# Kernel optimization log

Measured on AMD Instinct MI355X. Metric: run time of the kernel, lower is better.

Reference implementation:

```python
import jax, jax.numpy as jnp
import numpy as np
from jax import lax

B, SEQ, CIN = 8, 4096, 7
DM, NL, PL = 512, 4, 16
NP = SEQ // PL            # 256 patches
NS, DC, EXP = 16, 4, 2
DI = EXP * DM             # 1024 inner dim
DTR = (DM + 15) // 16     # 32 dt_rank (mamba_ssm default ceil(d_model/16))
CD, PRED = 64, 96
EPS = 1e-5


def setup_inputs() -> dict:
    key = jax.random.key(0)
    ks = jax.random.split(key, 16)
    r = lambda k, s, sc=0.02: jax.random.normal(k, s, jnp.float32) * sc
    A_row = jnp.arange(1, NS + 1, dtype=jnp.float32)
    return {
        "x": jax.random.normal(ks[0], (B, SEQ, CIN), jnp.float32),
        "in_g": jnp.ones((CIN,), jnp.float32), "in_b": jnp.zeros((CIN,), jnp.float32),
        "pe_W": r(ks[1], (DM, CIN, PL), 0.1), "pe_b": jnp.zeros((DM,), jnp.float32),
        "ln_g": jnp.ones((NL, DM), jnp.float32), "ln_b": jnp.zeros((NL, DM), jnp.float32),
        "W_in": r(ks[2], (NL, 2 * DI, DM)),
        "conv_W": r(ks[3], (NL, DI, 1, DC), 0.2), "conv_b": jnp.zeros((NL, DI), jnp.float32),
        "W_x": r(ks[4], (NL, DTR + 2 * NS, DI)),
        "W_dt": r(ks[5], (NL, DI, DTR), 0.1),
        "b_dt": jnp.full((NL, DI), -4.6, jnp.float32),  # softplus^-1(~0.01)
        "A_log": jnp.log(jnp.tile(A_row, (NL, DI, 1))),
        "Dskip": jnp.ones((NL, DI), jnp.float32),
        "W_out": r(ks[6], (NL, DM, DI)),
        "fn_g": jnp.ones((DM,), jnp.float32), "fn_b": jnp.zeros((DM,), jnp.float32),
        "hW1": r(ks[7], (2 * CD, DM * NP)), "hb1": jnp.zeros((2 * CD,), jnp.float32),
        "hW2": r(ks[8], (PRED, 2 * CD)), "hb2": jnp.zeros((PRED,), jnp.float32),
    }


def layernorm(x, g, b):
    m = jnp.mean(x, axis=-1, keepdims=True)
    v = jnp.mean((x - m) ** 2, axis=-1, keepdims=True)
    return (x - m) * lax.rsqrt(v + EPS) * g + b


def silu(x):
    return x * jax.nn.sigmoid(x)


def selective_scan(dA, dBx, C):
    # dA, dBx: (B, L, DI, N);  C: (B, L, N)  ->  y: (B, L, DI)
    def step(h, t):
        dA_t, dbx_t, c_t = t
        h = dA_t * h + dbx_t                      # (B, DI, N)
        y = jnp.einsum('bdn,bn->bd', h, c_t)
        return h, y
    h0 = jnp.zeros((dA.shape[0], DI, NS), dA.dtype)
    _, ys = lax.scan(step, h0, (dA.transpose(1, 0, 2, 3), dBx.transpose(1, 0, 2, 3), C.transpose(1, 0, 2)))
    return ys.transpose(1, 0, 2)


def mamba_block(u, W_in, cW, cb, W_x, W_dt, b_dt, A_log, Dv, W_out):
    xz = jnp.einsum('bld,ed->ble', u, W_in)       # (B, L, 2*DI)
    xi, z = jnp.split(xz, 2, axis=-1)
    # causal depthwise conv over time
    xc = lax.conv_general_dilated(xi.transpose(0, 2, 1), cW, (1,), [(DC - 1, 0)],
                                  feature_group_count=DI,
                                  dimension_numbers=('NCH', 'OIH', 'NCH'))
    xc = silu(xc + cb[None, :, None]).transpose(0, 2, 1)  # (B, L, DI)
    dbl = jnp.einsum('bld,ed->ble', xc, W_x)      # (B, L, DTR + 2*NS)
    dt, Bm, Cm = dbl[..., :DTR], dbl[..., DTR:DTR + NS], dbl[..., DTR + NS:]
    delta = jax.nn.softplus(jnp.einsum('blr,dr->bld', dt, W_dt) + b_dt)  # (B, L, DI)
    A = -jnp.exp(A_log)                           # (DI, NS)
    dA = jnp.exp(delta[..., None] * A)            # (B, L, DI, NS)
    dBx = delta[..., None] * Bm[:, :, None, :] * xc[..., None]
    y = selective_scan(dA, dBx, Cm)
    y = (y + xc * Dv) * silu(z)
    return jnp.einsum('bld,od->blo', y, W_out)


def reference(x, in_g, in_b, pe_W, pe_b, ln_g, ln_b, W_in, conv_W, conv_b,
              W_x, W_dt, b_dt, A_log, Dskip, W_out, fn_g, fn_b, hW1, hb1, hW2, hb2):
    h = layernorm(x, in_g, in_b)
    # patch embed: stride==kernel Conv1d == per-patch matmul
    p = h.reshape(B, NP, PL, CIN)
    h = jnp.einsum('bnpc,dcp->bnd', p, pe_W) + pe_b   # (B, NP, DM)
    for i in range(NL):
        res = h
        h = layernorm(h, ln_g[i], ln_b[i])
        h = mamba_block(h, W_in[i], conv_W[i], conv_b[i], W_x[i], W_dt[i],
                        b_dt[i], A_log[i], Dskip[i], W_out[i])
        h = h + res                                   # dropout is identity at eval
    h = layernorm(h, fn_g, fn_b)
    h = h.reshape(B, -1)                              # (B, DM*NP)
    h = jax.nn.gelu(h @ hW1.T + hb1, approximate=False)
    return h @ hW2.T + hb2                            # (B, PRED)
```

## Files before the change

### kernel.cpp

```cpp
#include <hip/hip_runtime.h>
#include <hip/hip_bf16.h>
#include <math.h>

#define B_    8
#define SEQ_  4096
#define CIN_  7
#define DM_   512
#define NL_   4
#define PL_   16
#define NP_   256
#define NS_   16
#define DC_   4
#define DI_   1024
#define DTR_  32
#define CD_   64
#define PRED_ 96
#define TOK_  (B_*NP_)
#define KTOT_ (DM_*NP_)
#define EPS_  1e-5f
#define CL_   16
#define NCH_  (NP_/CL_)

typedef unsigned short u16;
typedef __attribute__((ext_vector_type(8))) short short8;
typedef __attribute__((ext_vector_type(4))) float floatx4;

__device__ __forceinline__ float silu_f(float x){ return x / (1.f + __expf(-x)); }
__device__ __forceinline__ float softplus_f(float x){ return x > 20.f ? x : log1pf(__expf(x)); }
__device__ __forceinline__ u16 f2bf(float f){
  union { __hip_bfloat16 h; u16 u; } cv; cv.h = __float2bfloat16(f); return cv.u;
}
__device__ __forceinline__ float bf2f(u16 u){
  union { unsigned int i; float f; } cv; cv.i = ((unsigned int)u) << 16; return cv.f;
}
#define GLDS16(g, l) __builtin_amdgcn_global_load_lds( \
    (const __attribute__((address_space(1))) void*)(g), \
    (__attribute__((address_space(3))) void*)(l), 16, 0, 0)

__global__ void ln7_kernel(const float* __restrict__ x, const float* __restrict__ g,
                           const float* __restrict__ b, u16* __restrict__ xpb){
  int i = blockIdx.x*256 + threadIdx.x;
  if (i >= B_*SEQ_) return;
  float v[CIN_]; float m = 0.f;
  #pragma unroll
  for (int c=0;c<CIN_;c++){ v[c]=x[i*CIN_+c]; m+=v[c]; }
  m *= (1.f/CIN_);
  float var = 0.f;
  #pragma unroll
  for (int c=0;c<CIN_;c++){ float d=v[c]-m; var+=d*d; }
  var *= (1.f/CIN_);
  float r = rsqrtf(var + EPS_);
  int bn = i >> 4, p = i & 15;
  u16* row = xpb + (size_t)bn*128;
  #pragma unroll
  for (int c=0;c<CIN_;c++) row[c*16+p] = f2bf((v[c]-m)*r*g[c]+b[c]);
  row[112+p] = 0;
}

__global__ __launch_bounds__(256) void ln512_kernel(const float* __restrict__ in,
    const float* __restrict__ g, const float* __restrict__ b, u16* __restrict__ outb){
  int tid = threadIdx.x;
  int wv = tid>>6, lane = tid&63;
  int t = blockIdx.x*4 + wv;
  const float4* row = (const float4*)(in + (size_t)t*DM_);
  float4 v0 = row[lane], v1 = row[64+lane];
  float s = v0.x+v0.y+v0.z+v0.w + v1.x+v1.y+v1.z+v1.w;
  #pragma unroll
  for (int o=1;o<64;o<<=1) s += __shfl_xor(s,o);
  float m = s*(1.f/DM_);
  float d0x=v0.x-m,d0y=v0.y-m,d0z=v0.z-m,d0w=v0.w-m;
  float d1x=v1.x-m,d1y=v1.y-m,d1z=v1.z-m,d1w=v1.w-m;
  float q = d0x*d0x+d0y*d0y+d0z*d0z+d0w*d0w + d1x*d1x+d1y*d1y+d1z*d1z+d1w*d1w;
  #pragma unroll
  for (int o=1;o<64;o<<=1) q += __shfl_xor(q,o);
  float r = rsqrtf(q*(1.f/DM_) + EPS_);
  float4 g0 = ((const float4*)g)[lane], g1 = ((const float4*)g)[64+lane];
  float4 b0 = ((const float4*)b)[lane], b1 = ((const float4*)b)[64+lane];
  float4 o0 = { d0x*r*g0.x+b0.x, d0y*r*g0.y+b0.y, d0z*r*g0.z+b0.z, d0w*r*g0.w+b0.w };
  float4 o1 = { d1x*r*g1.x+b1.x, d1y*r*g1.y+b1.y, d1z*r*g1.z+b1.z, d1w*r*g1.w+b1.w };
  ushort4 p0 = { f2bf(o0.x), f2bf(o0.y), f2bf(o0.z), f2bf(o0.w) };
  ushort4 p1 = { f2bf(o1.x), f2bf(o1.y), f2bf(o1.z), f2bf(o1.w) };
  ((ushort4*)(outb + (size_t)t*DM_))[lane]    = p0;
  ((ushort4*)(outb + (size_t)t*DM_))[64+lane] = p1;
}

template<int BM, int BN, bool ACC, bool BIAS>
__global__ __launch_bounds__(256) void gemm_bf16(const u16* __restrict__ A,
    const u16* __restrict__ Bw, float* __restrict__ C, const float* __restrict__ bias,
    int K, int lda, int ldb, int ldc){
  constexpr int MI = BM/32, NI = BN/32;
  __shared__ __align__(16) u16 As[BM*64];
  __shared__ __align__(16) u16 Bs[BN*64];
  int tid = threadIdx.x;
  int wave = __builtin_amdgcn_readfirstlane(tid>>6);
  int lane = tid&63;
  int wm = wave>>1, wn = wave&1;
  int quad = lane>>4, l16 = lane&15;
  int bm = blockIdx.y*BM, bn = blockIdx.x*BN;
  int r8 = lane>>3, sseg = lane&7;
  int gseg = sseg ^ r8;
  floatx4 acc[MI][NI] = {};
  for (int k0 = 0; k0 < K; k0 += 64){
    #pragma unroll
    for (int r = 0; r < BM/32; r++){
      int rowb = (r*4 + wave)*8;
      const u16* gp = A + (size_t)(bm + rowb + r8)*lda + k0 + gseg*8;
      GLDS16(gp, &As[rowb*64]);
    }
    #pragma unroll
    for (int r = 0; r < BN/32; r++){
      int rowb = (r*4 + wave)*8;
      const u16* gp = Bw + (size_t)(bn + rowb + r8)*ldb + k0 + gseg*8;
      GLDS16(gp, &Bs[rowb*64]);
    }
    __syncthreads();
    #pragma unroll
    for (int kh = 0; kh < 2; kh++){
      short8 af[MI], bfr[NI];
      #pragma unroll
      for (int i = 0; i < MI; i++){
        int row = wm*(BM/2)+i*16+l16;
        af[i] = *(short8*)&As[row*64 + (((kh*4+quad)^(row&7))*8)];
      }
      #pragma unroll
      for (int j = 0; j < NI; j++){
        int row = wn*(BN/2)+j*16+l16;
        bfr[j] = *(short8*)&Bs[row*64 + (((kh*4+quad)^(row&7))*8)];
      }
      #pragma unroll
      for (int i = 0; i < MI; i++)
        #pragma unroll
        for (int j = 0; j < NI; j++)
          acc[i][j] = __builtin_amdgcn_mfma_f32_16x16x32_bf16(af[i], bfr[j], acc[i][j], 0, 0, 0);
    }
    __syncthreads();
  }
  #pragma unroll
  for (int i = 0; i < MI; i++){
    #pragma unroll
    for (int j = 0; j < NI; j++){
      #pragma unroll
      for (int r = 0; r < 4; r++){
        int m  = bm + wm*(BM/2) + i*16 + quad*4 + r;
        int nn = bn + wn*(BN/2) + j*16 + l16;
        float v = acc[i][j][r];
        if (ACC) C[(size_t)m*ldc+nn] += v;
        else     C[(size_t)m*ldc+nn]  = BIAS ? v + bias[nn] : v;
      }
    }
  }
}

__global__ __launch_bounds__(256) void dblpart_kernel(const u16* __restrict__ A,
    const u16* __restrict__ Bw, float* __restrict__ part){
  __shared__ __align__(16) u16 As[64*64];
  __shared__ __align__(16) u16 Bs[64*64];
  int tid = threadIdx.x;
  int wave = __builtin_amdgcn_readfirstlane(tid>>6);
  int lane = tid&63;
  int wm = wave>>1, wn = wave&1;
  int quad = lane>>4, l16 = lane&15;
  int bm = blockIdx.x*64;
  int kc = blockIdx.y;
  int r8 = lane>>3, sseg = lane&7;
  int gseg = sseg ^ r8;
  floatx4 acc[2][2] = {};
  for (int k0 = kc*256; k0 < kc*256 + 256; k0 += 64){
    #pragma unroll
    for (int r = 0; r < 2; r++){
      int rowb = (r*4 + wave)*8;
      GLDS16(A  + (size_t)(bm + rowb + r8)*DI_ + k0 + gseg*8, &As[rowb*64]);
      GLDS16(Bw + (size_t)(     rowb + r8)*DI_ + k0 + gseg*8, &Bs[rowb*64]);
    }
    __syncthreads();
    #pragma unroll
    for (int kh = 0; kh < 2; kh++){
      short8 af[2], bfr[2];
      #pragma unroll
      for (int i = 0; i < 2; i++){
        int row = wm*32+i*16+l16;
        af[i] = *(short8*)&As[row*64 + (((kh*4+quad)^(row&7))*8)];
      }
      #pragma unroll
      for (int j = 0; j < 2; j++){
        int row = wn*32+j*16+l16;
        bfr[j] = *(short8*)&Bs[row*64 + (((kh*4+quad)^(row&7))*8)];
      }
      #pragma unroll
      for (int i = 0; i < 2; i++)
        #pragma unroll
        for (int j = 0; j < 2; j++)
          acc[i][j] = __builtin_amdgcn_mfma_f32_16x16x32_bf16(af[i], bfr[j], acc[i][j], 0, 0, 0);
    }
    __syncthreads();
  }
  float* dst = part + (size_t)kc*TOK_*64;
  #pragma unroll
  for (int i = 0; i < 2; i++)
    #pragma unroll
    for (int j = 0; j < 2; j++)
      #pragma unroll
      for (int r = 0; r < 4; r++){
        int m  = bm + wm*32 + i*16 + quad*4 + r;
        int nn = wn*32 + j*16 + l16;
        dst[(size_t)m*64+nn] = acc[i][j][r];
      }
}

__global__ void conv_silu_kernel(const float* __restrict__ xz, const float* __restrict__ cW,
                                 const float* __restrict__ cb, u16* __restrict__ xcb){
  int idx = blockIdx.x*256 + threadIdx.x;
  if (idx >= TOK_*DI_/4) return;
  int c4 = idx & (DI_/4 - 1); int t = idx >> 8;
  int l = t & (NP_-1);
  int c = c4*4;
  float4 acc = *(const float4*)&cb[c];
  float wa[4], wb[4], wc[4], wd[4];
  *(float4*)wa = *(const float4*)&cW[(c+0)*DC_];
  *(float4*)wb = *(const float4*)&cW[(c+1)*DC_];
  *(float4*)wc = *(const float4*)&cW[(c+2)*DC_];
  *(float4*)wd = *(const float4*)&cW[(c+3)*DC_];
  const float* base = xz + (size_t)t*(2*DI_) + c;
  #pragma unroll
  for (int k = 0; k < DC_; k++){
    if (l - 3 + k >= 0){
      float4 xv = *(const float4*)(base + (k-3)*(2*DI_));
      acc.x += xv.x*wa[k];
      acc.y += xv.y*wb[k];
      acc.z += xv.z*wc[k];
      acc.w += xv.w*wd[k];
    }
  }
  ushort4 pb = { f2bf(silu_f(acc.x)), f2bf(silu_f(acc.y)),
                 f2bf(silu_f(acc.z)), f2bf(silu_f(acc.w)) };
  *(ushort4*)&xcb[(size_t)t*DI_ + c] = pb;
}

__global__ __launch_bounds__(256) void delta_kernel(const float* __restrict__ part,
    const float* __restrict__ wdtT, const float* __restrict__ bdt,
    float* __restrict__ dbl, float* __restrict__ delta){
  __shared__ float sdt[16][DTR_];
  int tid = threadIdx.x;
  int t0 = blockIdx.y*16;
  int dx = blockIdx.x;
  int d = dx*256 + tid;
  for (int i = tid; i < 16*32; i += 256){
    int t = i >> 5, r = i & 31;
    size_t o = (size_t)(t0 + t)*64 + r;
    sdt[t][r] = part[o] + part[(size_t)TOK_*64 + o]
              + part[(size_t)2*TOK_*64 + o] + part[(size_t)3*TOK_*64 + o];
  }
  if (dx == 0){
    for (int i = tid; i < 16*32; i += 256){
      int t = i >> 5, c = i & 31;
      size_t o = (size_t)(t0 + t)*64 + 32 + c;
      dbl[o] = part[o] + part[(size_t)TOK_*64 + o]
             + part[(size_t)2*TOK_*64 + o] + part[(size_t)3*TOK_*64 + o];
    }
  }
  float wv[DTR_];
  #pragma unroll
  for (int r = 0; r < DTR_; r++) wv[r] = wdtT[(size_t)r*DI_ + d];
  float bb = bdt[d];
  __syncthreads();
  #pragma unroll 4
  for (int t = 0; t < 16; t++){
    float acc = bb;
    #pragma unroll
    for (int r = 0; r < DTR_; r++) acc += sdt[t][r]*wv[r];
    delta[(size_t)(t0 + t)*DI_ + d] = softplus_f(acc);
  }
}

__global__ __launch_bounds__(256) void scan_part_kernel(const float* __restrict__ delta,
    const u16* __restrict__ xcb, const float* __restrict__ dbl,
    const float* __restrict__ Alog, float* __restrict__ hend, float* __restrict__ aprod){
  __shared__ float sBC[CL_][32];
  int tid = threadIdx.x;
  int d = blockIdx.x*256 + tid;
  int bych = blockIdx.y;
  int b = bych >> 4, ch = bych & (NCH_-1);
  int base = b*NP_ + ch*CL_;
  for (int i = tid; i < CL_*32; i += 256){
    int t = i >> 5, c = i & 31;
    sBC[t][c] = dbl[(size_t)(base+t)*64 + 32 + c];
  }
  float A[NS_], h[NS_], pr[NS_];
  #pragma unroll
  for (int k = 0; k < NS_; k++){
    A[k] = -__expf(Alog[(size_t)d*NS_ + k]);
    h[k] = 0.f; pr[k] = 1.f;
  }
  __syncthreads();
  #pragma unroll
  for (int t = 0; t < CL_; t++){
    int row = base + t;
    float de = delta[(size_t)row*DI_ + d];
    float xv = bf2f(xcb[(size_t)row*DI_ + d]);
    float cde = de*xv;
    #pragma unroll
    for (int k = 0; k < NS_; k++){
      float a = __expf(de*A[k]);
      h[k] = a*h[k] + cde*sBC[t][k];
      pr[k] *= a;
    }
  }
  size_t o = ((size_t)bych*DI_ + d)*NS_;
  #pragma unroll
  for (int k = 0; k < NS_; k++){ hend[o+k] = h[k]; aprod[o+k] = pr[k]; }
}

__global__ __launch_bounds__(256) void scan_fix_kernel(const float* __restrict__ aprod,
    float* __restrict__ hend){
  int id = blockIdx.x*256 + threadIdx.x;
  int nd = id & (DI_*NS_ - 1);
  int b  = id >> 14;
  float h = 0.f;
  #pragma unroll
  for (int ch = 0; ch < NCH_; ch++){
    size_t idx = (size_t)(b*NCH_ + ch)*(DI_*NS_) + nd;
    float ap = aprod[idx];
    float he = hend[idx];
    hend[idx] = h;
    h = ap*h + he;
  }
}

__global__ __launch_bounds__(256) void scan_final_kernel(const float* __restrict__ delta,
    const u16* __restrict__ xcb, const float* __restrict__ dbl,
    const float* __restrict__ xz, const float* __restrict__ Dv,
    const float* __restrict__ Alog, const float* __restrict__ hin,
    u16* __restrict__ yb){
  __shared__ float sBC[CL_][32];
  int tid = threadIdx.x;
  int d = blockIdx.x*256 + tid;
  int bych = blockIdx.y;
  int b = bych >> 4, ch = bych & (NCH_-1);
  int base = b*NP_ + ch*CL_;
  for (int i = tid; i < CL_*32; i += 256){
    int t = i >> 5, c = i & 31;
    sBC[t][c] = dbl[(size_t)(base+t)*64 + 32 + c];
  }
  float A[NS_], h[NS_];
  size_t o = ((size_t)bych*DI_ + d)*NS_;
  #pragma unroll
  for (int k = 0; k < NS_; k++){
    A[k] = -__expf(Alog[(size_t)d*NS_ + k]);
    h[k] = hin[o + k];
  }
  float Dvd = Dv[d];
  __syncthreads();
  #pragma unroll
  for (int t = 0; t < CL_; t++){
    int row = base + t;
    float de = delta[(size_t)row*DI_ + d];
    float xv = bf2f(xcb[(size_t)row*DI_ + d]);
    float zz = xz[(size_t)row*(2*DI_) + DI_ + d];
    float cde = de*xv;
    float p = 0.f;
    #pragma unroll
    for (int k = 0; k < NS_; k++){
      float a = __expf(de*A[k]);
      h[k] = a*h[k] + cde*sBC[t][k];
      p += h[k]*sBC[t][16+k];
    }
    yb[(size_t)row*DI_ + d] = f2bf((p + xv*Dvd) * silu_f(zz));
  }
}

__global__ __launch_bounds__(256) void head1_kernel(const float* __restrict__ hW1,
    const u16* __restrict__ ub, float* __restrict__ partial){
  __shared__ __align__(16) u16 As[128*64];
  __shared__ __align__(16) u16 Bs[16*64];
  int tid = threadIdx.x;
  int wave = __builtin_amdgcn_readfirstlane(tid>>6);
  int lane = tid & 63, quad = lane>>4, l16 = lane&15;
  int kc = blockIdx.x;
  int arow = tid & 127, apair = tid >> 7;
  floatx4 acc[2] = {};
  for (int sc = 0; sc < 4; sc++){
    int k0 = kc*256 + sc*64;
    const float* ap = hW1 + (size_t)arow*KTOT_ + k0 + apair*32;
    #pragma unroll
    for (int s = 0; s < 4; s++){
      float4 f0 = *(const float4*)(ap + s*8);
      float4 f1 = *(const float4*)(ap + s*8 + 4);
      union { u16 h[8]; int4 v; } pk;
      pk.h[0]=f2bf(f0.x); pk.h[1]=f2bf(f0.y); pk.h[2]=f2bf(f0.z); pk.h[3]=f2bf(f0.w);
      pk.h[4]=f2bf(f1.x); pk.h[5]=f2bf(f1.y); pk.h[6]=f2bf(f1.z); pk.h[7]=f2bf(f1.w);
      int seg = apair*4 + s;
      *(int4*)&As[arow*64 + ((seg^(arow&7))*8)] = pk.v;
    }
    if (tid < 128){
      int brow = tid >> 3, bseg = tid & 7;
      int4 bv = {0,0,0,0};
      if (brow < 8) bv = *(const int4*)&ub[(size_t)brow*KTOT_ + k0 + bseg*8];
      *(int4*)&Bs[brow*64 + ((bseg^(brow&7))*8)] = bv;
    }
    __syncthreads();
    #pragma unroll
    for (int kh = 0; kh < 2; kh++){
      short8 bf = *(short8*)&Bs[l16*64 + (((kh*4+quad)^(l16&7))*8)];
      #pragma unroll
      for (int i = 0; i < 2; i++){
        int row = wave*32 + i*16 + l16;
        short8 af = *(short8*)&As[row*64 + (((kh*4+quad)^(row&7))*8)];
        acc[i] = __builtin_amdgcn_mfma_f32_16x16x32_bf16(af, bf, acc[i], 0, 0, 0);
      }
    }
    __syncthreads();
  }
  if (l16 < 8){
    #pragma unroll
    for (int i = 0; i < 2; i++)
      #pragma unroll
      for (int r = 0; r < 4; r++){
        int n = wave*32 + i*16 + quad*4 + r;
        partial[(size_t)kc*1024 + n*8 + l16] = acc[i][r];
      }
  }
}

__global__ void head_comb1_kernel(const float* __restrict__ partial, float* __restrict__ pp2){
  int out = blockIdx.x*256 + threadIdx.x;
  int g = blockIdx.y;
  const float* p = partial + (size_t)g*64*1024 + out;
  float s = 0.f;
  #pragma unroll 8
  for (int j = 0; j < 64; j++) s += p[(size_t)j*1024];
  pp2[g*1024 + out] = s;
}

__global__ void head_comb2_kernel(const float* __restrict__ pp2,
    const float* __restrict__ hb1, float* __restrict__ t1){
  int out = blockIdx.x*256 + threadIdx.x;
  int n = out >> 3, m = out & 7;
  float s = hb1[n];
  #pragma unroll
  for (int g = 0; g < 8; g++) s += pp2[g*1024 + out];
  float ge = 0.5f*s*(1.f + erff(s*0.70710678118f));
  t1[m*128 + n] = ge;
}

__global__ void head2_kernel(const float* __restrict__ t1, const float* __restrict__ hW2,
                             const float* __restrict__ hb2, float* __restrict__ out){
  int idx = blockIdx.x*128 + threadIdx.x;
  if (idx >= B_*PRED_) return;
  int m = idx / PRED_, q = idx % PRED_;
  float s = hb2[q];
  #pragma unroll 16
  for (int k = 0; k < 2*CD_; k++) s += t1[m*128 + k]*hW2[q*128 + k];
  out[idx] = s;
}

__global__ __launch_bounds__(256) void prep_kernel(const float* __restrict__ W_dt,
    const float* __restrict__ W_x, const float* __restrict__ W_in,
    const float* __restrict__ W_out, const float* __restrict__ peW,
    float* __restrict__ wdtT, u16* __restrict__ wxB,
    u16* __restrict__ WinB, u16* __restrict__ WoutB, u16* __restrict__ peWb){
  int idx = blockIdx.x*256 + threadIdx.x;
  {
    float4 v = ((const float4*)W_in)[idx];
    ushort4 o = { f2bf(v.x), f2bf(v.y), f2bf(v.z), f2bf(v.w) };
    ((ushort4*)WinB)[idx] = o;
  }
  if (idx < 524288){
    float4 v = ((const float4*)W_out)[idx];
    ushort4 o = { f2bf(v.x), f2bf(v.y), f2bf(v.z), f2bf(v.w) };
    ((ushort4*)WoutB)[idx] = o;
  }
  if (idx < NL_*64*DI_/4){
    float4 v = ((const float4*)W_x)[idx];
    ushort4 o = { f2bf(v.x), f2bf(v.y), f2bf(v.z), f2bf(v.w) };
    ((ushort4*)wxB)[idx] = o;
  }
  if (idx < NL_*DTR_*DI_){
    int l = idx / (DTR_*DI_); int rem = idx % (DTR_*DI_);
    int r = rem / DI_; int d = rem % DI_;
    wdtT[idx] = W_dt[((size_t)l*DI_ + d)*DTR_ + r];
  }
  if (idx < 512*128){
    int d = idx >> 7, kk = idx & 127;
    peWb[idx] = (kk < 112) ? f2bf(peW[d*112 + kk]) : (u16)0;
  }
}

extern "C" void kernel_launch(void* const* d_in, const int* in_sizes, int n_in,
                              void* d_out, int out_size, void* d_ws, size_t ws_size,
                              hipStream_t stream) {
  const float* x      = (const float*)d_in[0];
  const float* in_g   = (const float*)d_in[1];
  const float* in_b   = (const float*)d_in[2];
  const float* pe_W   = (const float*)d_in[3];
  const float* pe_b   = (const float*)d_in[4];
  const float* ln_g   = (const float*)d_in[5];
  const float* ln_b   = (const float*)d_in[6];
  const float* W_in   = (const float*)d_in[7];
  const float* conv_W = (const float*)d_in[8];
  const float* conv_b = (const float*)d_in[9];
  const float* W_x    = (const float*)d_in[10];
  const float* W_dt   = (const float*)d_in[11];
  const float* b_dt   = (const float*)d_in[12];
  const float* A_log  = (const float*)d_in[13];
  const float* Dskip  = (const float*)d_in[14];
  const float* W_out  = (const float*)d_in[15];
  const float* fn_g   = (const float*)d_in[16];
  const float* fn_b   = (const float*)d_in[17];
  const float* hW1    = (const float*)d_in[18];
  const float* hb1    = (const float*)d_in[19];
  const float* hW2    = (const float*)d_in[20];
  const float* hb2    = (const float*)d_in[21];

  float* ws    = (float*)d_ws;
  float* h     = ws;
  float* un    = h     + 1048576;
  float* xz    = un    + 1048576;
  float* xc    = xz    + 4194304;
  float* dblb  = xc    + 2097152;
  float* delta = dblb  + 131072;
  float* y     = delta + 2097152;
  float* wdtT  = y     + 2097152;
  u16*   wxB   = (u16*)(wdtT + 131072);
  float* bf_rgn= wdtT + 131072 + 131072;
  u16*   unb   = (u16*)bf_rgn;
  u16*   yb    = (u16*)(bf_rgn + 524288);
  u16*   WinB  = (u16*)(bf_rgn + 524288 + 1048576);
  u16*   WoutB = (u16*)(bf_rgn + 524288 + 1048576 + 2097152);
  u16*   peWb  = (u16*)(bf_rgn + 524288 + 1048576 + 2097152 + 1048576);
  float* aprod = bf_rgn + 524288 + 1048576 + 2097152 + 1048576 + 32768;
  float* hend  = y;
  u16*   xcb   = (u16*)xc;
  u16*   xpb   = (u16*)y;
  float* dblpart = aprod;
  float* partial = xz;
  float* pp2     = xz + 524288;
  float* t1      = xz + 532480;

  prep_kernel<<<4096, 256, 0, stream>>>(W_dt, W_x, W_in, W_out, pe_W,
                                        wdtT, wxB, WinB, WoutB, peWb);
  ln7_kernel<<<(B_*SEQ_+255)/256, 256, 0, stream>>>(x, in_g, in_b, xpb);
  gemm_bf16<64,128,false,true><<<dim3(DM_/128, TOK_/64), 256, 0, stream>>>(
      xpb, peWb, h, pe_b, 128, 128, 128, DM_);

  for (int l = 0; l < NL_; l++){
    ln512_kernel<<<TOK_/4, 256, 0, stream>>>(h, ln_g + l*DM_, ln_b + l*DM_, unb);
    gemm_bf16<64,128,false,false><<<dim3(2*DI_/128, TOK_/64), 256, 0, stream>>>(
        unb, WinB + (size_t)l*2*DI_*DM_, xz, nullptr, DM_, DM_, DM_, 2*DI_);
    conv_silu_kernel<<<(TOK_*DI_/4)/256, 256, 0, stream>>>(
        xz, conv_W + (size_t)l*DI_*DC_, conv_b + (size_t)l*DI_, xcb);
    dblpart_kernel<<<dim3(TOK_/64, 4), 256, 0, stream>>>(
        xcb, wxB + (size_t)l*64*DI_, dblpart);
    delta_kernel<<<dim3(DI_/256, TOK_/16), 256, 0, stream>>>(
        dblpart, wdtT + (size_t)l*DTR_*DI_, b_dt + (size_t)l*DI_, dblb, delta);
    scan_part_kernel<<<dim3(DI_/256, B_*NCH_), 256, 0, stream>>>(
        delta, xcb, dblb, A_log + (size_t)l*DI_*NS_, hend, aprod);
    scan_fix_kernel<<<(B_*DI_*NS_)/256, 256, 0, stream>>>(aprod, hend);
    scan_final_kernel<<<dim3(DI_/256, B_*NCH_), 256, 0, stream>>>(
        delta, xcb, dblb, xz, Dskip + (size_t)l*DI_, A_log + (size_t)l*DI_*NS_, hend, yb);
    gemm_bf16<64,64,true,false><<<dim3(DM_/64, TOK_/64), 256, 0, stream>>>(
        yb, WoutB + (size_t)l*DM_*DI_, h, nullptr, DI_, DI_, DI_, DM_);
  }

  ln512_kernel<<<TOK_/4, 256, 0, stream>>>(h, fn_g, fn_b, unb);
  head1_kernel<<<512, 256, 0, stream>>>(hW1, unb, partial);
  head_comb1_kernel<<<dim3(4, 8), 256, 0, stream>>>(partial, pp2);
  head_comb2_kernel<<<4, 256, 0, stream>>>(pp2, hb1, t1);
  head2_kernel<<<6, 128, 0, stream>>>(t1, hW2, hb2, (float*)d_out);
}
```

Baseline: 553.1 us.

## Fuse conv+SiLU into x_proj GEMM and delta projection into chunk scan

Computes the causal depthwise conv and SiLU directly into the shared-memory A tile of the x_proj partial GEMM, so the block no longer reloads xc from global. The delta projection is merged into the first chunked-scan pass, keeping delta in registers instead of re-reading it. It also widens the in_proj GEMM M tile to 128 and moves the dblpart buffer to a different scratch region. Together these remove two launches per layer and some global round trips, at the cost of larger shared memory per block and more registers.

```diff
diff --git a/kernel.cpp b/kernel.cpp
--- a/kernel.cpp
+++ b/kernel.cpp
@@ -151,39 +151,83 @@
   }
 }
 
-__global__ __launch_bounds__(256) void dblpart_kernel(const u16* __restrict__ A,
-    const u16* __restrict__ Bw, float* __restrict__ part){
-  __shared__ __align__(16) u16 As[64*64];
+__global__ __launch_bounds__(256) void convdbl_kernel(const float* __restrict__ xz,
+    const float* __restrict__ cW, const float* __restrict__ cb,
+    const u16* __restrict__ wxB, u16* __restrict__ xcb, float* __restrict__ part){
+  __shared__ __align__(16) u16 As[64*256];
   __shared__ __align__(16) u16 Bs[64*64];
   int tid = threadIdx.x;
+  int t0 = blockIdx.x*64;
+  int kc = blockIdx.y;
+  int cbase = kc*256;
+  {
+    int cg = tid & 31;
+    int tq = tid >> 5;
+    int c = cbase + cg*8;
+    float wt[8][4], bias[8];
+    #pragma unroll
+    for (int j = 0; j < 8; j++){
+      float4 w4 = *(const float4*)&cW[(size_t)(c+j)*DC_];
+      wt[j][0]=w4.x; wt[j][1]=w4.y; wt[j][2]=w4.z; wt[j][3]=w4.w;
+    }
+    float4 bq0 = *(const float4*)&cb[c], bq1 = *(const float4*)&cb[c+4];
+    bias[0]=bq0.x; bias[1]=bq0.y; bias[2]=bq0.z; bias[3]=bq0.w;
+    bias[4]=bq1.x; bias[5]=bq1.y; bias[6]=bq1.z; bias[7]=bq1.w;
+    #pragma unroll
+    for (int r = 0; r < 8; r++){
+      int trow = t0 + r*8 + tq;
+      int l = trow & (NP_-1);
+      float a[8];
+      #pragma unroll
+      for (int j = 0; j < 8; j++) a[j] = bias[j];
+      #pragma unroll
+      for (int tap = 0; tap < DC_; tap++){
+        if (l + tap >= 3){
+          const float* px = xz + (size_t)(trow + tap - 3)*(2*DI_) + c;
+          float4 x0 = *(const float4*)px;
+          float4 x1 = *(const float4*)(px + 4);
+          a[0]+=x0.x*wt[0][tap]; a[1]+=x0.y*wt[1][tap];
+          a[2]+=x0.z*wt[2][tap]; a[3]+=x0.w*wt[3][tap];
+          a[4]+=x1.x*wt[4][tap]; a[5]+=x1.y*wt[5][tap];
+          a[6]+=x1.z*wt[6][tap]; a[7]+=x1.w*wt[7][tap];
+        }
+      }
+      union { u16 h[8]; int4 v; } pk;
+      #pragma unroll
+      for (int j = 0; j < 8; j++) pk.h[j] = f2bf(silu_f(a[j]));
+      int trel = trow - t0;
+      *(int4*)&As[trel*256 + ((cg ^ (trel&7))*8)] = pk.v;
+      *(int4*)&xcb[(size_t)trow*DI_ + c] = pk.v;
+    }
+  }
+  __syncthreads();
   int wave = __builtin_amdgcn_readfirstlane(tid>>6);
   int lane = tid&63;
   int wm = wave>>1, wn = wave&1;
   int quad = lane>>4, l16 = lane&15;
-  int bm = blockIdx.x*64;
-  int kc = blockIdx.y;
   int r8 = lane>>3, sseg = lane&7;
   int gseg = sseg ^ r8;
   floatx4 acc[2][2] = {};
-  for (int k0 = kc*256; k0 < kc*256 + 256; k0 += 64){
+  for (int sc = 0; sc < 4; sc++){
+    int k0 = cbase + sc*64;
     #pragma unroll
     for (int r = 0; r < 2; r++){
       int rowb = (r*4 + wave)*8;
-      GLDS16(A  + (size_t)(bm + rowb + r8)*DI_ + k0 + gseg*8, &As[rowb*64]);
-      GLDS16(Bw + (size_t)(     rowb + r8)*DI_ + k0 + gseg*8, &Bs[rowb*64]);
+      GLDS16(wxB + (size_t)(rowb + r8)*DI_ + k0 + gseg*8, &Bs[rowb*64]);
     }
     __syncthreads();
     #pragma unroll
     for (int kh = 0; kh < 2; kh++){
+      int lseg = sc*8 + kh*4 + quad;
       short8 af[2], bfr[2];
       #pragma unroll
       for (int i = 0; i < 2; i++){
-        int row = wm*32+i*16+l16;
-        af[i] = *(short8*)&As[row*64 + (((kh*4+quad)^(row&7))*8)];
+        int row = wm*32 + i*16 + l16;
+        af[i] = *(short8*)&As[row*256 + ((lseg ^ (row&7))*8)];
       }
       #pragma unroll
       for (int j = 0; j < 2; j++){
-        int row = wn*32+j*16+l16;
+        int row = wn*32 + j*16 + l16;
         bfr[j] = *(short8*)&Bs[row*64 + (((kh*4+quad)^(row&7))*8)];
       }
       #pragma unroll
@@ -201,89 +245,45 @@
     for (int j = 0; j < 2; j++)
       #pragma unroll
       for (int r = 0; r < 4; r++){
-        int m  = bm + wm*32 + i*16 + quad*4 + r;
+        int m  = t0 + wm*32 + i*16 + quad*4 + r;
         int nn = wn*32 + j*16 + l16;
         dst[(size_t)m*64+nn] = acc[i][j][r];
       }
 }
 
-__global__ void conv_silu_kernel(const float* __restrict__ xz, const float* __restrict__ cW,
-                                 const float* __restrict__ cb, u16* __restrict__ xcb){
-  int idx = blockIdx.x*256 + threadIdx.x;
-  if (idx >= TOK_*DI_/4) return;
-  int c4 = idx & (DI_/4 - 1); int t = idx >> 8;
-  int l = t & (NP_-1);
-  int c = c4*4;
-  float4 acc = *(const float4*)&cb[c];
-  float wa[4], wb[4], wc[4], wd[4];
-  *(float4*)wa = *(const float4*)&cW[(c+0)*DC_];
-  *(float4*)wb = *(const float4*)&cW[(c+1)*DC_];
-  *(float4*)wc = *(const float4*)&cW[(c+2)*DC_];
-  *(float4*)wd = *(const float4*)&cW[(c+3)*DC_];
-  const float* base = xz + (size_t)t*(2*DI_) + c;
-  #pragma unroll
-  for (int k = 0; k < DC_; k++){
-    if (l - 3 + k >= 0){
-      float4 xv = *(const float4*)(base + (k-3)*(2*DI_));
-      acc.x += xv.x*wa[k];
-      acc.y += xv.y*wb[k];
-      acc.z += xv.z*wc[k];
-      acc.w += xv.w*wd[k];
-    }
-  }
-  ushort4 pb = { f2bf(silu_f(acc.x)), f2bf(silu_f(acc.y)),
-                 f2bf(silu_f(acc.z)), f2bf(silu_f(acc.w)) };
-  *(ushort4*)&xcb[(size_t)t*DI_ + c] = pb;
-}
-
-__global__ __launch_bounds__(256) void delta_kernel(const float* __restrict__ part,
+__global__ __launch_bounds__(256) void dscan_kernel(const float* __restrict__ part,
     const float* __restrict__ wdtT, const float* __restrict__ bdt,
-    float* __restrict__ dbl, float* __restrict__ delta){
-  __shared__ float sdt[16][DTR_];
+    const u16* __restrict__ xcb, const float* __restrict__ Alog,
+    float* __restrict__ dbl, float* __restrict__ delta,
+    float* __restrict__ hend, float* __restrict__ aprod){
+  __shared__ float sdt[CL_][32];
+  __shared__ float sBC[CL_][32];
   int tid = threadIdx.x;
-  int t0 = blockIdx.y*16;
   int dx = blockIdx.x;
+  int bych = blockIdx.y;
+  int t0 = bych*CL_;
+  for (int i = tid; i < CL_*64; i += 256){
+    int t = i >> 6, col = i & 63;
+    size_t o = (size_t)(t0+t)*64 + col;
+    float s = part[o] + part[(size_t)TOK_*64 + o]
+            + part[(size_t)2*TOK_*64 + o] + part[(size_t)3*TOK_*64 + o];
+    if (col < 32) sdt[t][col] = s;
+    else { sBC[t][col-32] = s; if (dx == 0) dbl[o] = s; }
+  }
   int d = dx*256 + tid;
-  for (int i = tid; i < 16*32; i += 256){
-    int t = i >> 5, r = i & 31;
-    size_t o = (size_t)(t0 + t)*64 + r;
-    sdt[t][r] = part[o] + part[(size_t)TOK_*64 + o]
-              + part[(size_t)2*TOK_*64 + o] + part[(size_t)3*TOK_*64 + o];
-  }
-  if (dx == 0){
-    for (int i = tid; i < 16*32; i += 256){
-      int t = i >> 5, c = i & 31;
-      size_t o = (size_t)(t0 + t)*64 + 32 + c;
-      dbl[o] = part[o] + part[(size_t)TOK_*64 + o]
-             + part[(size_t)2*TOK_*64 + o] + part[(size_t)3*TOK_*64 + o];
-    }
-  }
   float wv[DTR_];
   #pragma unroll
   for (int r = 0; r < DTR_; r++) wv[r] = wdtT[(size_t)r*DI_ + d];
   float bb = bdt[d];
   __syncthreads();
+  float de[CL_];
   #pragma unroll 4
-  for (int t = 0; t < 16; t++){
+  for (int t = 0; t < CL_; t++){
     float acc = bb;
     #pragma unroll
     for (int r = 0; r < DTR_; r++) acc += sdt[t][r]*wv[r];
-    delta[(size_t)(t0 + t)*DI_ + d] = softplus_f(acc);
-  }
-}
-
-__global__ __launch_bounds__(256) void scan_part_kernel(const float* __restrict__ delta,
-    const u16* __restrict__ xcb, const float* __restrict__ dbl,
-    const float* __restrict__ Alog, float* __restrict__ hend, float* __restrict__ aprod){
-  __shared__ float sBC[CL_][32];
-  int tid = threadIdx.x;
-  int d = blockIdx.x*256 + tid;
-  int bych = blockIdx.y;
-  int b = bych >> 4, ch = bych & (NCH_-1);
-  int base = b*NP_ + ch*CL_;
-  for (int i = tid; i < CL_*32; i += 256){
-    int t = i >> 5, c = i & 31;
-    sBC[t][c] = dbl[(size_t)(base+t)*64 + 32 + c];
+    de[t] = softplus_f(acc);
+    delta[(size_t)(t0+t)*DI_ + d] = de[t];
   }
   float A[NS_], h[NS_], pr[NS_];
   #pragma unroll
@@ -291,16 +291,13 @@
     A[k] = -__expf(Alog[(size_t)d*NS_ + k]);
     h[k] = 0.f; pr[k] = 1.f;
   }
-  __syncthreads();
   #pragma unroll
   for (int t = 0; t < CL_; t++){
-    int row = base + t;
-    float de = delta[(size_t)row*DI_ + d];
-    float xv = bf2f(xcb[(size_t)row*DI_ + d]);
-    float cde = de*xv;
+    float xv = bf2f(xcb[(size_t)(t0+t)*DI_ + d]);
+    float cde = de[t]*xv;
     #pragma unroll
     for (int k = 0; k < NS_; k++){
-      float a = __expf(de*A[k]);
+      float a = __expf(de[t]*A[k]);
       h[k] = a*h[k] + cde*sBC[t][k];
       pr[k] *= a;
     }
@@ -335,8 +332,7 @@
   int tid = threadIdx.x;
   int d = blockIdx.x*256 + tid;
   int bych = blockIdx.y;
-  int b = bych >> 4, ch = bych & (NCH_-1);
-  int base = b*NP_ + ch*CL_;
+  int base = bych*CL_;
   for (int i = tid; i < CL_*32; i += 256){
     int t = i >> 5, c = i & 31;
     sBC[t][c] = dbl[(size_t)(base+t)*64 + 32 + c];
@@ -531,7 +527,7 @@
   float* hend  = y;
   u16*   xcb   = (u16*)xc;
   u16*   xpb   = (u16*)y;
-  float* dblpart = aprod;
+  float* dblpart = un;
   float* partial = xz;
   float* pp2     = xz + 524288;
   float* t1      = xz + 532480;
@@ -544,16 +540,14 @@
 
   for (int l = 0; l < NL_; l++){
     ln512_kernel<<<TOK_/4, 256, 0, stream>>>(h, ln_g + l*DM_, ln_b + l*DM_, unb);
-    gemm_bf16<64,128,false,false><<<dim3(2*DI_/128, TOK_/64), 256, 0, stream>>>(
+    gemm_bf16<128,128,false,false><<<dim3(2*DI_/128, TOK_/128), 256, 0, stream>>>(
         unb, WinB + (size_t)l*2*DI_*DM_, xz, nullptr, DM_, DM_, DM_, 2*DI_);
-    conv_silu_kernel<<<(TOK_*DI_/4)/256, 256, 0, stream>>>(
-        xz, conv_W + (size_t)l*DI_*DC_, conv_b + (size_t)l*DI_, xcb);
-    dblpart_kernel<<<dim3(TOK_/64, 4), 256, 0, stream>>>(
-        xcb, wxB + (size_t)l*64*DI_, dblpart);
-    delta_kernel<<<dim3(DI_/256, TOK_/16), 256, 0, stream>>>(
-        dblpart, wdtT + (size_t)l*DTR_*DI_, b_dt + (size_t)l*DI_, dblb, delta);
-    scan_part_kernel<<<dim3(DI_/256, B_*NCH_), 256, 0, stream>>>(
-        delta, xcb, dblb, A_log + (size_t)l*DI_*NS_, hend, aprod);
+    convdbl_kernel<<<dim3(TOK_/64, 4), 256, 0, stream>>>(
+        xz, conv_W + (size_t)l*DI_*DC_, conv_b + (size_t)l*DI_,
+        wxB + (size_t)l*64*DI_, xcb, dblpart);
+    dscan_kernel<<<dim3(DI_/256, B_*NCH_), 256, 0, stream>>>(
+        dblpart, wdtT + (size_t)l*DTR_*DI_, b_dt + (size_t)l*DI_,
+        xcb, A_log + (size_t)l*DI_*NS_, dblb, delta, hend, aprod);
     scan_fix_kernel<<<(B_*DI_*NS_)/256, 256, 0, stream>>>(aprod, hend);
     scan_final_kernel<<<dim3(DI_/256, B_*NCH_), 256, 0, stream>>>(
         delta, xcb, dblb, xz, Dskip + (size_t)l*DI_, A_log + (size_t)l*DI_*NS_, hend, yb);
```

Result: no change. 560.5 us (+1.3%).
